# Kernel optimization log

Measured on AMD Instinct MI355X. Metric: run time of the kernel, lower is better.

The kernel has to match this reference:

```python
import jax, jax.numpy as jnp
import numpy as np

B, INPUT_DIM, EMB_DIM = 16384, 2048, 768
DOMAIN_NUM, MEMORY_NUM, TAU = 9, 10, 32.0


def setup_inputs() -> dict:
    key = jax.random.key(0)
    k1, k2, k3, k4, k5 = jax.random.split(key, 5)
    feature = jax.random.normal(k1, (B, INPUT_DIM), dtype=jnp.float32)
    category = jax.random.randint(k2, (B,), 0, DOMAIN_NUM, dtype=jnp.int64)
    # Linear(input_dim, emb_dim, bias=False) weights: [emb_dim, input_dim]
    W_topic = jax.random.normal(k3, (EMB_DIM, INPUT_DIM), dtype=jnp.float32) * 0.02
    W_domain = jax.random.normal(k4, (EMB_DIM, INPUT_DIM), dtype=jnp.float32) * 0.02
    # domain_num Embedding(memory_num, emb_dim) tables, stacked: [D, M, E]
    memory_tables = jax.random.normal(k5, (DOMAIN_NUM, MEMORY_NUM, EMB_DIM), dtype=jnp.float32)
    return {"feature": feature, "W_topic": W_topic, "W_domain": W_domain,
            "memory_tables": memory_tables, "category": category}


def reference(feature, W_topic, W_domain, memory_tables, category):
    eps = 1e-12
    # F.normalize(feature, p=2, dim=-1)
    norm = jnp.maximum(jnp.linalg.norm(feature, axis=-1, keepdims=True), eps)
    feat = feature / norm                                   # [B, I]
    # per-sample gather of each sample's category memory table: [B, M, E]
    mem = memory_tables[category]
    # faithful quirk: loop over domain_num indexes the BATCH dim of the stack
    D = memory_tables.shape[0]
    mems_d = mem[:D]                                        # [D, M, E]
    t = feat @ W_topic.T                                    # [B, E]
    topic_att = jax.nn.softmax(jnp.einsum('be,dme->bdm', t, mems_d) * TAU, axis=-1)
    sep = jnp.einsum('bdm,dme->bde', topic_att, mems_d)     # [B, D, E]
    dproj = feat @ W_domain.T                               # [B, E]
    domain_att = jax.nn.softmax(jnp.einsum('bde,be->bd', sep, dproj) * TAU, axis=-1)
    return domain_att[:, None, :]                           # [B, 1, D]
```

## Files before the change

kernel.cpp:

```cpp
#include <hip/hip_runtime.h>
#include <math.h>

#define TAU_F 32.0f

typedef __attribute__((ext_vector_type(8))) _Float16 half8;
typedef __attribute__((ext_vector_type(2))) __fp16 half2v;
typedef __attribute__((ext_vector_type(4))) float f32x4;

union HU { uint4 u; half8 v; };

__device__ __forceinline__ void sync_lds_only() {
    asm volatile("s_waitcnt lgkmcnt(0)" ::: "memory");
    __builtin_amdgcn_s_barrier();
}

__global__ __launch_bounds__(256) void gproj2(
    const float* __restrict__ Wt, const float* __restrict__ Wd,
    const float* __restrict__ mem, const int* __restrict__ cat,
    float* __restrict__ P)
{
    __shared__ float Ml[96 * 36];
    __shared__ float Wl[32 * 68];

    const int bid = blockIdx.x;
    const int mat = bid >> 7;
    const int ks  = (bid >> 5) & 3;
    const int ct  = bid & 31;
    const int c0  = ct * 64;
    const int tid = threadIdx.x;
    const float* __restrict__ W = mat ? Wd : Wt;

    const int tr = tid >> 4;
    const int tc = tid & 15;

    float acc[6][4];
    #pragma unroll
    for (int j = 0; j < 6; ++j)
        #pragma unroll
        for (int q = 0; q < 4; ++q) acc[j][q] = 0.f;

    for (int ch = 0; ch < 6; ++ch) {
        __syncthreads();
        #pragma unroll
        for (int p = 0; p < 3; ++p) {
            const int idx = tid + 256 * p;
            const int r   = idx >> 3;
            const int kq  = idx & 7;
            float4 v = make_float4(0.f, 0.f, 0.f, 0.f);
            if (r < 90) {
                const int d = r / 10;
                const int mrow = cat[d] * 10 + (r - d * 10);
                v = *(const float4*)(mem + (size_t)mrow * 768 + ks * 192 + ch * 32 + kq * 4);
            }
            *(float4*)(Ml + r * 36 + kq * 4) = v;
        }
        #pragma unroll
        for (int p = 0; p < 2; ++p) {
            const int idx = tid + 256 * p;
            const int e   = idx >> 4;
            const int c4  = (idx & 15) * 4;
            *(float4*)(Wl + e * 68 + c4) =
                *(const float4*)(W + (size_t)(ks * 192 + ch * 32 + e) * 2048 + c0 + c4);
        }
        __syncthreads();

        #pragma unroll
        for (int e = 0; e < 32; e += 4) {
            float4 m4[6], w4[4];
            #pragma unroll
            for (int j = 0; j < 6; ++j) m4[j] = *(const float4*)(Ml + (tr * 6 + j) * 36 + e);
            #pragma unroll
            for (int q = 0; q < 4; ++q) w4[q] = *(const float4*)(Wl + (e + q) * 68 + tc * 4);
            #pragma unroll
            for (int j = 0; j < 6; ++j) {
                const float mv[4] = {m4[j].x, m4[j].y, m4[j].z, m4[j].w};
                #pragma unroll
                for (int q = 0; q < 4; ++q) {
                    acc[j][0] = fmaf(mv[q], w4[q].x, acc[j][0]);
                    acc[j][1] = fmaf(mv[q], w4[q].y, acc[j][1]);
                    acc[j][2] = fmaf(mv[q], w4[q].z, acc[j][2]);
                    acc[j][3] = fmaf(mv[q], w4[q].w, acc[j][3]);
                }
            }
        }
    }

    #pragma unroll
    for (int j = 0; j < 6; ++j) {
        float4 v = make_float4(acc[j][0], acc[j][1], acc[j][2], acc[j][3]);
        *(float4*)(P + (size_t)ks * 393216 + (size_t)(mat * 96 + tr * 6 + j) * 2048 + c0 + tc * 4) = v;
    }
}

__global__ __launch_bounds__(256) void split_g3(
    const float* __restrict__ P, unsigned short* __restrict__ gB)
{
    const int u  = blockIdx.x * 256 + threadIdx.x;
    const int n  = u >> 8;
    const int k0 = (u & 255) * 8;

    float s[8] = {0.f, 0.f, 0.f, 0.f, 0.f, 0.f, 0.f, 0.f};
    #pragma unroll
    for (int ks = 0; ks < 4; ++ks) {
        const float4 a = *(const float4*)(P + (size_t)ks * 393216 + (size_t)n * 2048 + k0);
        const float4 b = *(const float4*)(P + (size_t)ks * 393216 + (size_t)n * 2048 + k0 + 4);
        s[0] += a.x; s[1] += a.y; s[2] += a.z; s[3] += a.w;
        s[4] += b.x; s[5] += b.y; s[6] += b.z; s[7] += b.w;
    }
    union { _Float16 h[8]; uint4 u4; } hi, lo;
    #pragma unroll
    for (int e = 0; e < 8; ++e) {
        const _Float16 h = (_Float16)s[e];
        hi.h[e] = h;
        lo.h[e] = (_Float16)(s[e] - (float)h);
    }
    const int kc = k0 >> 5;
    const int lq = (k0 >> 3) & 3;
    const int nq = n / 48;
    const int rm = n - nq * 48;
    const int j  = rm >> 4;
    const int lm = rm & 15;
    const size_t fH = (size_t)((kc * 12 + nq * 3 + j) * 2 + 0) * 512 + lq * 128 + lm * 8;
    const size_t fL = (size_t)((kc * 12 + nq * 3 + j) * 2 + 1) * 512 + lq * 128 + lm * 8;
    *(uint4*)(gB + fH) = hi.u4;
    *(uint4*)(gB + fL) = lo.u4;
}

#define SPAD 197

__global__ __launch_bounds__(256, 2) void fused_mfma7(
    const float* __restrict__ feat, const unsigned short* __restrict__ gB,
    float* __restrict__ out)
{
    __shared__ __align__(16) char smem[50688];
    __shared__ float ssqf[64];
    unsigned short* aS = (unsigned short*)smem;
    float* scores = (float*)smem;

    const int tid  = threadIdx.x;
    const int row0 = blockIdx.x * 64;
    const int w  = tid >> 6, l = tid & 63;
    const int lm = l & 15,  lq = l >> 4;
    const int nq = (w + blockIdx.x) & 3;
    const bool topic = (nq < 2);

    const int srow = tid >> 3;
    const int skf  = (tid & 7) * 4;

    f32x4 acc[4][3];
    #pragma unroll
    for (int i = 0; i < 4; ++i)
        #pragma unroll
        for (int j = 0; j < 3; ++j) acc[i][j] = (f32x4)0.f;
    float ssq0 = 0.f, ssq1 = 0.f;

    const float* fb0 = feat + (size_t)(row0 + srow) * 2048 + skf;
    const float* fb1 = feat + (size_t)(row0 + 32 + srow) * 2048 + skf;
    const unsigned short* bbase = gB + nq * 3072 + l * 8;

    auto cw = [&](int buf, float4 va, float4 vb) {
        union { half2v h2[2]; uint2 u2; } h0, l0, h1, l1;
        ssq0 = fmaf(va.x, va.x, ssq0); ssq0 = fmaf(va.y, va.y, ssq0);
        ssq0 = fmaf(va.z, va.z, ssq0); ssq0 = fmaf(va.w, va.w, ssq0);
        ssq1 = fmaf(vb.x, vb.x, ssq1); ssq1 = fmaf(vb.y, vb.y, ssq1);
        ssq1 = fmaf(vb.z, vb.z, ssq1); ssq1 = fmaf(vb.w, vb.w, ssq1);
        half2v a01 = __builtin_amdgcn_cvt_pkrtz(va.x, va.y);
        half2v a23 = __builtin_amdgcn_cvt_pkrtz(va.z, va.w);
        h0.h2[0] = a01; h0.h2[1] = a23;
        l0.h2[0] = __builtin_amdgcn_cvt_pkrtz(va.x - (float)a01[0], va.y - (float)a01[1]);
        l0.h2[1] = __builtin_amdgcn_cvt_pkrtz(va.z - (float)a23[0], va.w - (float)a23[1]);
        half2v b01 = __builtin_amdgcn_cvt_pkrtz(vb.x, vb.y);
        half2v b23 = __builtin_amdgcn_cvt_pkrtz(vb.z, vb.w);
        h1.h2[0] = b01; h1.h2[1] = b23;
        l1.h2[0] = __builtin_amdgcn_cvt_pkrtz(vb.x - (float)b01[0], vb.y - (float)b01[1]);
        l1.h2[1] = __builtin_amdgcn_cvt_pkrtz(vb.z - (float)b23[0], vb.w - (float)b23[1]);
        unsigned short* pH = aS + (size_t)((buf * 2 + 0) * 64) * 40;
        unsigned short* pL = aS + (size_t)((buf * 2 + 1) * 64) * 40;
        *(uint2*)(pH + srow * 40 + skf)        = h0.u2;
        *(uint2*)(pH + (srow + 32) * 40 + skf) = h1.u2;
        *(uint2*)(pL + srow * 40 + skf)        = l0.u2;
        *(uint2*)(pL + (srow + 32) * 40 + skf) = l1.u2;
    };

    float4 a00 = *(const float4*)(fb0);
    float4 a01 = *(const float4*)(fb1);
    float4 a10 = *(const float4*)(fb0 + 32);
    float4 a11 = *(const float4*)(fb1 + 32);
    uint4 bh[3], bl[3];
    #pragma unroll
    for (int j = 0; j < 3; ++j) bh[j] = *(const uint4*)(bbase + j * 1024);
    if (topic) {
        #pragma unroll
        for (int j = 0; j < 3; ++j) bl[j] = *(const uint4*)(bbase + j * 1024 + 512);
    }
    cw(0, a00, a01);
    sync_lds_only();

    for (int kc = 0; kc < 64; ++kc) {
        const int kb = (kc + 1 < 64) ? kc + 1 : 63;
        uint4 bhn[3], bln[3];
        #pragma unroll
        for (int j = 0; j < 3; ++j)
            bhn[j] = *(const uint4*)(bbase + (size_t)kb * 12288 + j * 1024);
        if (topic) {
            #pragma unroll
            for (int j = 0; j < 3; ++j)
                bln[j] = *(const uint4*)(bbase + (size_t)kb * 12288 + j * 1024 + 512);
        }
        const int ka = (kc + 2 < 64) ? kc + 2 : 63;
        float4 fa0 = *(const float4*)(fb0 + ka * 32);
        float4 fa1 = *(const float4*)(fb1 + ka * 32);

        if (kc < 63) cw((kc + 1) & 1, a10, a11);

        const int cb = kc & 1;
        half8 fh[4], fl[4];
        #pragma unroll
        for (int i = 0; i < 4; ++i) {
            HU th;
            th.u = *(const uint4*)(aS + (size_t)((cb * 2 + 0) * 64 + i * 16 + lm) * 40 + lq * 8);
            fh[i] = th.v;
        }
        if (topic) {
            #pragma unroll
            for (int i = 0; i < 4; ++i) {
                HU tl;
                tl.u = *(const uint4*)(aS + (size_t)((cb * 2 + 1) * 64 + i * 16 + lm) * 40 + lq * 8);
                fl[i] = tl.v;
            }
        }

        if (topic) {
            #pragma unroll
            for (int j = 0; j < 3; ++j) {
                HU h8, l8; h8.u = bh[j]; l8.u = bl[j];
                #pragma unroll
                for (int i = 0; i < 4; ++i) {
                    acc[i][j] = __builtin_amdgcn_mfma_f32_16x16x32_f16(fh[i], h8.v, acc[i][j], 0, 0, 0);
                    acc[i][j] = __builtin_amdgcn_mfma_f32_16x16x32_f16(fh[i], l8.v, acc[i][j], 0, 0, 0);
                    acc[i][j] = __builtin_amdgcn_mfma_f32_16x16x32_f16(fl[i], h8.v, acc[i][j], 0, 0, 0);
                }
            }
        } else {
            #pragma unroll
            for (int j = 0; j < 3; ++j) {
                HU h8; h8.u = bh[j];
                #pragma unroll
                for (int i = 0; i < 4; ++i)
                    acc[i][j] = __builtin_amdgcn_mfma_f32_16x16x32_f16(fh[i], h8.v, acc[i][j], 0, 0, 0);
            }
        }

        sync_lds_only();

        a10 = fa0; a11 = fa1;
        #pragma unroll
        for (int j = 0; j < 3; ++j) bh[j] = bhn[j];
        if (topic) {
            #pragma unroll
            for (int j = 0; j < 3; ++j) bl[j] = bln[j];
        }
    }

    ssq0 += __shfl_xor(ssq0, 1, 64); ssq1 += __shfl_xor(ssq1, 1, 64);
    ssq0 += __shfl_xor(ssq0, 2, 64); ssq1 += __shfl_xor(ssq1, 2, 64);
    ssq0 += __shfl_xor(ssq0, 4, 64); ssq1 += __shfl_xor(ssq1, 4, 64);
    if ((tid & 7) == 0) { ssqf[srow] = ssq0; ssqf[32 + srow] = ssq1; }
    __syncthreads();

    #pragma unroll
    for (int i = 0; i < 4; ++i)
        #pragma unroll
        for (int j = 0; j < 3; ++j)
            #pragma unroll
            for (int r = 0; r < 4; ++r)
                scores[(size_t)(i * 16 + lq * 4 + r) * SPAD + nq * 48 + j * 16 + lm] = acc[i][j][r];
    __syncthreads();

    if (tid < 64) {
        const int r = tid;
        const float inv = TAU_F / fmaxf(sqrtf(ssqf[r]), 1e-12f);
        const float* sc = scores + (size_t)r * SPAD;
        float lg[9];
        float dmax = -1e30f;
        #pragma unroll
        for (int d = 0; d < 9; ++d) {
            const float* v = sc + d * 10;
            const float* u = sc + 96 + d * 10;
            float mx = v[0];
            #pragma unroll
            for (int m = 1; m < 10; ++m) mx = fmaxf(mx, v[m]);
            float ssum = 0.f, dot = 0.f;
            #pragma unroll
            for (int m = 0; m < 10; ++m) {
                const float p = __expf((v[m] - mx) * inv);
                ssum += p;
                dot = fmaf(p, u[m], dot);
            }
            const float lgt = (dot / ssum) * inv;
            lg[d] = lgt;
            dmax = fmaxf(dmax, lgt);
        }
        float s2 = 0.f;
        #pragma unroll
        for (int d = 0; d < 9; ++d) { const float p = __expf(lg[d] - dmax); lg[d] = p; s2 += p; }
        const float r2 = 1.0f / s2;
        #pragma unroll
        for (int d = 0; d < 9; ++d)
            out[(size_t)(row0 + r) * 9 + d] = lg[d] * r2;
    }
}

extern "C" void kernel_launch(void* const* d_in, const int* in_sizes, int n_in,
                              void* d_out, int out_size, void* d_ws, size_t ws_size,
                              hipStream_t stream) {
    const float* feature = (const float*)d_in[0];
    const float* Wt      = (const float*)d_in[1];
    const float* Wd      = (const float*)d_in[2];
    const float* mem     = (const float*)d_in[3];
    const int*   cat     = (const int*)d_in[4];

    float* P  = (float*)d_ws;
    unsigned short* gB = (unsigned short*)((char*)d_ws + 50331648);
    float* out = (float*)d_out;

    gproj2<<<256, 256, 0, stream>>>(Wt, Wd, mem, cat, P);
    split_g3<<<192, 256, 0, stream>>>(P, gB);
    fused_mfma7<<<256, 256, 0, stream>>>(feature, gB, out);
}
```

Measured before the change: 255.4 us.

## Split K dimension across four blocks and add reduction epilogue kernel

The fused GEMM-plus-softmax kernel is split along the 2048-wide reduction dimension into four K-slices, launching 1024 blocks instead of 256. Each block writes partial scores and partial squared norms to workspace, and a new epilogue kernel sums the partials and applies the two softmaxes. The goal is more parallelism across the GPU's compute units, helped by smaller shared memory and launch bounds that allow four blocks per CU. The cost is extra global traffic for the partial results and one more kernel launch. P2 reuses the workspace region that already holds P.

```diff
diff --git a/kernel.cpp b/kernel.cpp
--- a/kernel.cpp
+++ b/kernel.cpp
@@ -126,19 +126,17 @@
     *(uint4*)(gB + fL) = lo.u4;
 }
 
-#define SPAD 197
-
-__global__ __launch_bounds__(256, 2) void fused_mfma7(
+__global__ __launch_bounds__(256, 4) void fused_mfma8(
     const float* __restrict__ feat, const unsigned short* __restrict__ gB,
-    float* __restrict__ out)
+    float* __restrict__ P2, float* __restrict__ ssqp)
 {
-    __shared__ __align__(16) char smem[50688];
-    __shared__ float ssqf[64];
-    unsigned short* aS = (unsigned short*)smem;
-    float* scores = (float*)smem;
-
-    const int tid  = threadIdx.x;
-    const int row0 = blockIdx.x * 64;
+    __shared__ __align__(16) unsigned short aS[4 * 64 * 40];
+
+    const int tid = threadIdx.x;
+    const int rt  = blockIdx.x >> 2;
+    const int ks  = blockIdx.x & 3;
+    const int row0 = rt * 64;
+
     const int w  = tid >> 6, l = tid & 63;
     const int lm = l & 15,  lq = l >> 4;
     const int nq = (w + blockIdx.x) & 3;
@@ -154,9 +152,9 @@
         for (int j = 0; j < 3; ++j) acc[i][j] = (f32x4)0.f;
     float ssq0 = 0.f, ssq1 = 0.f;
 
-    const float* fb0 = feat + (size_t)(row0 + srow) * 2048 + skf;
-    const float* fb1 = feat + (size_t)(row0 + 32 + srow) * 2048 + skf;
-    const unsigned short* bbase = gB + nq * 3072 + l * 8;
+    const float* fb0 = feat + (size_t)(row0 + srow) * 2048 + ks * 512 + skf;
+    const float* fb1 = feat + (size_t)(row0 + 32 + srow) * 2048 + ks * 512 + skf;
+    const unsigned short* bbase = gB + (size_t)ks * 196608 + nq * 3072 + l * 8;
 
     auto cw = [&](int buf, float4 va, float4 vb) {
         union { half2v h2[2]; uint2 u2; } h0, l0, h1, l1;
@@ -196,8 +194,8 @@
     cw(0, a00, a01);
     sync_lds_only();
 
-    for (int kc = 0; kc < 64; ++kc) {
-        const int kb = (kc + 1 < 64) ? kc + 1 : 63;
+    for (int kc = 0; kc < 16; ++kc) {
+        const int kb = (kc + 1 < 16) ? kc + 1 : 15;
         uint4 bhn[3], bln[3];
         #pragma unroll
         for (int j = 0; j < 3; ++j)
@@ -207,11 +205,11 @@
             for (int j = 0; j < 3; ++j)
                 bln[j] = *(const uint4*)(bbase + (size_t)kb * 12288 + j * 1024 + 512);
         }
-        const int ka = (kc + 2 < 64) ? kc + 2 : 63;
+        const int ka = (kc + 2 < 16) ? kc + 2 : 15;
         float4 fa0 = *(const float4*)(fb0 + ka * 32);
         float4 fa1 = *(const float4*)(fb1 + ka * 32);
 
-        if (kc < 63) cw((kc + 1) & 1, a10, a11);
+        if (kc < 15) cw((kc + 1) & 1, a10, a11);
 
         const int cb = kc & 1;
         half8 fh[4], fl[4];
@@ -265,8 +263,10 @@
     ssq0 += __shfl_xor(ssq0, 1, 64); ssq1 += __shfl_xor(ssq1, 1, 64);
     ssq0 += __shfl_xor(ssq0, 2, 64); ssq1 += __shfl_xor(ssq1, 2, 64);
     ssq0 += __shfl_xor(ssq0, 4, 64); ssq1 += __shfl_xor(ssq1, 4, 64);
-    if ((tid & 7) == 0) { ssqf[srow] = ssq0; ssqf[32 + srow] = ssq1; }
-    __syncthreads();
+    if ((tid & 7) == 0) {
+        ssqp[(size_t)ks * 16384 + row0 + srow]      = ssq0;
+        ssqp[(size_t)ks * 16384 + row0 + 32 + srow] = ssq1;
+    }
 
     #pragma unroll
     for (int i = 0; i < 4; ++i)
@@ -274,19 +274,56 @@
         for (int j = 0; j < 3; ++j)
             #pragma unroll
             for (int r = 0; r < 4; ++r)
-                scores[(size_t)(i * 16 + lq * 4 + r) * SPAD + nq * 48 + j * 16 + lm] = acc[i][j][r];
+                P2[((size_t)ks * 16384 + row0 + i * 16 + lq * 4 + r) * 192 + nq * 48 + j * 16 + lm]
+                    = acc[i][j][r];
+}
+
+#define EP_SPAD 196
+__global__ __launch_bounds__(256) void ep_kernel(
+    const float* __restrict__ P2, const float* __restrict__ ssqp,
+    float* __restrict__ out)
+{
+    __shared__ float sc[64 * EP_SPAD];
+    const int tid  = threadIdx.x;
+    const int row0 = blockIdx.x * 64;
+
+    float4 s[12];
+    #pragma unroll
+    for (int p = 0; p < 12; ++p) s[p] = make_float4(0.f, 0.f, 0.f, 0.f);
+    #pragma unroll
+    for (int ks = 0; ks < 4; ++ks)
+        #pragma unroll
+        for (int p = 0; p < 12; ++p) {
+            const int u   = p * 256 + tid;
+            const int row = u / 48;
+            const int c4  = (u - row * 48) * 4;
+            const float4 v = *(const float4*)(P2 + ((size_t)ks * 16384 + row0 + row) * 192 + c4);
+            s[p].x += v.x; s[p].y += v.y; s[p].z += v.z; s[p].w += v.w;
+        }
+    #pragma unroll
+    for (int p = 0; p < 12; ++p) {
+        const int u   = p * 256 + tid;
+        const int row = u / 48;
+        const int c4  = (u - row * 48) * 4;
+        *(float4*)(sc + row * EP_SPAD + c4) = s[p];
+    }
+    float nsq = 0.f;
+    if (tid < 64) {
+        nsq = ssqp[row0 + tid] + ssqp[16384 + row0 + tid]
+            + ssqp[32768 + row0 + tid] + ssqp[49152 + row0 + tid];
+    }
     __syncthreads();
 
     if (tid < 64) {
         const int r = tid;
-        const float inv = TAU_F / fmaxf(sqrtf(ssqf[r]), 1e-12f);
-        const float* sc = scores + (size_t)r * SPAD;
+        const float inv = TAU_F / fmaxf(sqrtf(nsq), 1e-12f);
+        const float* scr = sc + (size_t)r * EP_SPAD;
         float lg[9];
         float dmax = -1e30f;
         #pragma unroll
         for (int d = 0; d < 9; ++d) {
-            const float* v = sc + d * 10;
-            const float* u = sc + 96 + d * 10;
+            const float* v = scr + d * 10;
+            const float* u = scr + 96 + d * 10;
             float mx = v[0];
             #pragma unroll
             for (int m = 1; m < 10; ++m) mx = fmaxf(mx, v[m]);
@@ -320,11 +357,14 @@
     const float* mem     = (const float*)d_in[3];
     const int*   cat     = (const int*)d_in[4];
 
+    float* P2 = (float*)d_ws;
     float* P  = (float*)d_ws;
     unsigned short* gB = (unsigned short*)((char*)d_ws + 50331648);
+    float* ssqp = (float*)((char*)d_ws + 50331648 + 1572864);
     float* out = (float*)d_out;
 
     gproj2<<<256, 256, 0, stream>>>(Wt, Wd, mem, cat, P);
     split_g3<<<192, 256, 0, stream>>>(P, gB);
-    fused_mfma7<<<256, 256, 0, stream>>>(feature, gB, out);
-}
+    fused_mfma8<<<1024, 256, 0, stream>>>(feature, gB, P2, ssqp);
+    ep_kernel<<<256, 256, 0, stream>>>(P2, ssqp, out);
+}
```

Result: slower. 351.9 us (+37.8%).
